# Performance work log

Measured on AMD Instinct MI355X. Metric: run time of the kernel, lower is better.

The kernel has to match this reference:

```python
import jax, jax.numpy as jnp
import numpy as np

MARGIN = 1.0
EPS = 1e-6


def _cos(a, b):
    # Row-wise cosine similarity, matching torch.nn.CosineSimilarity semantics:
    # dot / max(||a|| * ||b||, eps)
    num = jnp.sum(a * b, axis=-1)
    den = jnp.maximum(jnp.linalg.norm(a, axis=-1) * jnp.linalg.norm(b, axis=-1), EPS)
    return num / den


def setup_inputs() -> dict:
    key = jax.random.key(0)
    k1, k2, k3 = jax.random.split(key, 3)
    B, D = 16384, 1024
    output = jax.random.normal(k1, (B, D), dtype=jnp.float32)
    target = jax.random.normal(k2, (B, D), dtype=jnp.float32)
    # offset in [0, B-1); j = (i + 1 + neg_idx) % B guarantees j != i, uniform over the rest
    neg_idx = jax.random.randint(k3, (B,), 0, B - 1, dtype=jnp.int64)
    return {"output": output, "target": target, "neg_idx": neg_idx}


def reference(output, target, neg_idx):
    B = output.shape[0]
    j = (jnp.arange(B) + 1 + neg_idx) % B  # random negative index, j != i
    t_neg = target[j]                       # gather negative label embeddings [B, D]
    hinge = jax.nn.relu(MARGIN - _cos(target, output) + _cos(t_neg, output))
    return jnp.sum(hinge) / B
```

## Files before the change

### kernel.cpp

```cpp
#include <hip/hip_runtime.h>
#include <hip/hip_bf16.h>


#define EPS 1e-6f

typedef float f4 __attribute__((ext_vector_type(4)));

#define DPP_STEP(x, ctrl, rm, bm)                                             \
    x += __int_as_float(__builtin_amdgcn_update_dpp(                          \
        0, __float_as_int(x), (ctrl), (rm), (bm), true))

__device__ __forceinline__ float dpp_wave_sum(float x) {
    DPP_STEP(x, 0x111, 0xf, 0xf);
    DPP_STEP(x, 0x112, 0xf, 0xf);
    DPP_STEP(x, 0x114, 0xf, 0xe);
    DPP_STEP(x, 0x118, 0xf, 0xc);
    DPP_STEP(x, 0x142, 0xa, 0xf);
    DPP_STEP(x, 0x143, 0xc, 0xf);
    return x;
}

struct RowBuf {
    f4 o[4], t[4], n[4];
};

__device__ __forceinline__ void issue_loads(RowBuf& rb,
                                            const float* __restrict__ outm,
                                            const float* __restrict__ tgt,
                                            int i, int j, int lane, int D) {
    const f4* o4 = (const f4*)(outm + (size_t)i * D);
    const f4* t4 = (const f4*)(tgt  + (size_t)i * D);
    const f4* n4 = (const f4*)(tgt  + (size_t)j * D);
#pragma unroll
    for (int k = 0; k < 4; ++k)
        rb.o[k] = __builtin_nontemporal_load(&o4[lane + 64 * k]);
#pragma unroll
    for (int k = 0; k < 4; ++k) rb.t[k] = t4[lane + 64 * k];
#pragma unroll
    for (int k = 0; k < 4; ++k) rb.n[k] = n4[lane + 64 * k];
}

__device__ __forceinline__ float consume(const RowBuf& rb) {
    float dto = 0.f, dno = 0.f, oo = 0.f, tt = 0.f, nn = 0.f;
#pragma unroll
    for (int k = 0; k < 4; ++k) {
        dto += rb.o[k].x*rb.t[k].x + rb.o[k].y*rb.t[k].y + rb.o[k].z*rb.t[k].z + rb.o[k].w*rb.t[k].w;
        dno += rb.o[k].x*rb.n[k].x + rb.o[k].y*rb.n[k].y + rb.o[k].z*rb.n[k].z + rb.o[k].w*rb.n[k].w;
        oo  += rb.o[k].x*rb.o[k].x + rb.o[k].y*rb.o[k].y + rb.o[k].z*rb.o[k].z + rb.o[k].w*rb.o[k].w;
        tt  += rb.t[k].x*rb.t[k].x + rb.t[k].y*rb.t[k].y + rb.t[k].z*rb.t[k].z + rb.t[k].w*rb.t[k].w;
        nn  += rb.n[k].x*rb.n[k].x + rb.n[k].y*rb.n[k].y + rb.n[k].z*rb.n[k].z + rb.n[k].w*rb.n[k].w;
    }
    dto = dpp_wave_sum(dto);
    dno = dpp_wave_sum(dno);
    oo  = dpp_wave_sum(oo);
    tt  = dpp_wave_sum(tt);
    nn  = dpp_wave_sum(nn);
    float no = sqrtf(oo);
    float h  = 1.f - dto / fmaxf(sqrtf(tt) * no, EPS)
                   + dno / fmaxf(sqrtf(nn) * no, EPS);
    return fmaxf(h, 0.f);
}

__global__ __launch_bounds__(256, 4) void hinge_cos_kernel(
    const float* __restrict__ outm,
    const float* __restrict__ tgt,
    const int*   __restrict__ negidx,
    float* __restrict__ res,
    int B, int D, float invB) {

    const int lane  = threadIdx.x & 63;
    const int wave  = threadIdx.x >> 6;
    const int wpb   = blockDim.x >> 6;
    const int gwave = blockIdx.x * wpb + wave;
    const int nwav  = gridDim.x * wpb;

    float acc = 0.f;

    RowBuf cur, nxt;
    int i = gwave;
    if (i < B) {
        int j = i + 1 + negidx[i];
        if (j >= B) j -= B;
        issue_loads(cur, outm, tgt, i, j, lane, D);
    }
    while (i < B) {
        const int inext = i + nwav;
        const bool havenext = inext < B;
        if (havenext) {
            int jn = inext + 1 + negidx[inext];
            if (jn >= B) jn -= B;
            issue_loads(nxt, outm, tgt, inext, jn, lane, D);
        }
        float h = consume(cur);
        if (lane == 63) acc += h;
        if (havenext) cur = nxt;
        i = inext;
    }

    __shared__ float red[4];
    if (lane == 63) red[wave] = acc;
    __syncthreads();
    if (threadIdx.x == 0) {
        float s = 0.f;
#pragma unroll
        for (int w = 0; w < 4; ++w) s += red[w];
        atomicAdd(res, s * invB);
    }
}

extern "C" void kernel_launch(void* const* d_in, const int* in_sizes, int n_in,
                              void* d_out, int out_size, void* d_ws, size_t ws_size,
                              hipStream_t stream) {
    const float* outm   = (const float*)d_in[0];
    const float* tgt    = (const float*)d_in[1];
    const int*   negidx = (const int*)d_in[2];
    float* res = (float*)d_out;

    const int B = in_sizes[2];
    const int D = in_sizes[0] / B;

    (void)hipMemsetAsync(res, 0, sizeof(float), stream);

    hinge_cos_kernel<<<1024, 256, 0, stream>>>(outm, tgt, negidx, res, B, D,
                                               1.0f / (float)B);
}
```

Measured before the change: 141.9 us.

## Replace register double-buffering with higher occupancy and prefetched neg index

Drops the explicit next-row register double buffer and instead loads the current row's vectors directly, prefetching only the next negative index. This cuts register pressure, which allows launch bounds of 8 blocks per CU and a grid of 2048 blocks, so more waves hide memory latency. The trade-off is that each wave no longer overlaps its own next-row loads with the current compute, and relies on the hardware scheduler across more waves instead. The scalar hinge math is now limited to lane 63.

```diff
diff --git a/kernel.cpp b/kernel.cpp
--- a/kernel.cpp
+++ b/kernel.cpp
@@ -20,48 +20,7 @@
     return x;
 }
 
-struct RowBuf {
-    f4 o[4], t[4], n[4];
-};
-
-__device__ __forceinline__ void issue_loads(RowBuf& rb,
-                                            const float* __restrict__ outm,
-                                            const float* __restrict__ tgt,
-                                            int i, int j, int lane, int D) {
-    const f4* o4 = (const f4*)(outm + (size_t)i * D);
-    const f4* t4 = (const f4*)(tgt  + (size_t)i * D);
-    const f4* n4 = (const f4*)(tgt  + (size_t)j * D);
-#pragma unroll
-    for (int k = 0; k < 4; ++k)
-        rb.o[k] = __builtin_nontemporal_load(&o4[lane + 64 * k]);
-#pragma unroll
-    for (int k = 0; k < 4; ++k) rb.t[k] = t4[lane + 64 * k];
-#pragma unroll
-    for (int k = 0; k < 4; ++k) rb.n[k] = n4[lane + 64 * k];
-}
-
-__device__ __forceinline__ float consume(const RowBuf& rb) {
-    float dto = 0.f, dno = 0.f, oo = 0.f, tt = 0.f, nn = 0.f;
-#pragma unroll
-    for (int k = 0; k < 4; ++k) {
-        dto += rb.o[k].x*rb.t[k].x + rb.o[k].y*rb.t[k].y + rb.o[k].z*rb.t[k].z + rb.o[k].w*rb.t[k].w;
-        dno += rb.o[k].x*rb.n[k].x + rb.o[k].y*rb.n[k].y + rb.o[k].z*rb.n[k].z + rb.o[k].w*rb.n[k].w;
-        oo  += rb.o[k].x*rb.o[k].x + rb.o[k].y*rb.o[k].y + rb.o[k].z*rb.o[k].z + rb.o[k].w*rb.o[k].w;
-        tt  += rb.t[k].x*rb.t[k].x + rb.t[k].y*rb.t[k].y + rb.t[k].z*rb.t[k].z + rb.t[k].w*rb.t[k].w;
-        nn  += rb.n[k].x*rb.n[k].x + rb.n[k].y*rb.n[k].y + rb.n[k].z*rb.n[k].z + rb.n[k].w*rb.n[k].w;
-    }
-    dto = dpp_wave_sum(dto);
-    dno = dpp_wave_sum(dno);
-    oo  = dpp_wave_sum(oo);
-    tt  = dpp_wave_sum(tt);
-    nn  = dpp_wave_sum(nn);
-    float no = sqrtf(oo);
-    float h  = 1.f - dto / fmaxf(sqrtf(tt) * no, EPS)
-                   + dno / fmaxf(sqrtf(nn) * no, EPS);
-    return fmaxf(h, 0.f);
-}
-
-__global__ __launch_bounds__(256, 4) void hinge_cos_kernel(
+__global__ __launch_bounds__(256, 8) void hinge_cos_kernel(
     const float* __restrict__ outm,
     const float* __restrict__ tgt,
     const int*   __restrict__ negidx,
@@ -70,30 +29,64 @@
 
     const int lane  = threadIdx.x & 63;
     const int wave  = threadIdx.x >> 6;
-    const int wpb   = blockDim.x >> 6;
-    const int gwave = blockIdx.x * wpb + wave;
-    const int nwav  = gridDim.x * wpb;
+    const int gwave = blockIdx.x * 4 + wave;
+    const int nwav  = gridDim.x * 4;
 
     float acc = 0.f;
 
-    RowBuf cur, nxt;
     int i = gwave;
+    int jcur = 0;
     if (i < B) {
-        int j = i + 1 + negidx[i];
-        if (j >= B) j -= B;
-        issue_loads(cur, outm, tgt, i, j, lane, D);
+        jcur = i + 1 + negidx[i];
+        if (jcur >= B) jcur -= B;
     }
+
     while (i < B) {
         const int inext = i + nwav;
-        const bool havenext = inext < B;
-        if (havenext) {
-            int jn = inext + 1 + negidx[inext];
-            if (jn >= B) jn -= B;
-            issue_loads(nxt, outm, tgt, inext, jn, lane, D);
+
+        int jn_raw = 0;
+        if (inext < B) jn_raw = negidx[inext];
+
+        const f4* o4 = (const f4*)(outm + (size_t)i * D);
+        const f4* t4 = (const f4*)(tgt  + (size_t)i * D);
+        const f4* n4 = (const f4*)(tgt  + (size_t)jcur * D);
+
+        f4 o[4], t[4], n[4];
+#pragma unroll
+        for (int k = 0; k < 4; ++k)
+            o[k] = __builtin_nontemporal_load(&o4[lane + 64 * k]);
+#pragma unroll
+        for (int k = 0; k < 4; ++k) t[k] = t4[lane + 64 * k];
+#pragma unroll
+        for (int k = 0; k < 4; ++k) n[k] = n4[lane + 64 * k];
+
+        int jnext = inext + 1 + jn_raw;
+        if (jnext >= B) jnext -= B;
+
+        float dto = 0.f, dno = 0.f, oo = 0.f, tt = 0.f, nn = 0.f;
+#pragma unroll
+        for (int k = 0; k < 4; ++k) {
+            dto += o[k].x*t[k].x + o[k].y*t[k].y + o[k].z*t[k].z + o[k].w*t[k].w;
+            dno += o[k].x*n[k].x + o[k].y*n[k].y + o[k].z*n[k].z + o[k].w*n[k].w;
+            oo  += o[k].x*o[k].x + o[k].y*o[k].y + o[k].z*o[k].z + o[k].w*o[k].w;
+            tt  += t[k].x*t[k].x + t[k].y*t[k].y + t[k].z*t[k].z + t[k].w*t[k].w;
+            nn  += n[k].x*n[k].x + n[k].y*n[k].y + n[k].z*n[k].z + n[k].w*n[k].w;
         }
-        float h = consume(cur);
-        if (lane == 63) acc += h;
-        if (havenext) cur = nxt;
+
+        dto = dpp_wave_sum(dto);
+        dno = dpp_wave_sum(dno);
+        oo  = dpp_wave_sum(oo);
+        tt  = dpp_wave_sum(tt);
+        nn  = dpp_wave_sum(nn);
+
+        if (lane == 63) {
+            float no = sqrtf(oo);
+            float h  = 1.f - dto / fmaxf(sqrtf(tt) * no, EPS)
+                           + dno / fmaxf(sqrtf(nn) * no, EPS);
+            acc += fmaxf(h, 0.f);
+        }
+
+        jcur = jnext;
         i = inext;
     }
 
@@ -121,6 +114,6 @@
 
     (void)hipMemsetAsync(res, 0, sizeof(float), stream);
 
-    hinge_cos_kernel<<<1024, 256, 0, stream>>>(outm, tgt, negidx, res, B, D,
+    hinge_cos_kernel<<<2048, 256, 0, stream>>>(outm, tgt, negidx, res, B, D,
                                                1.0f / (float)B);
 }
```

Result: slower. 152.5 us (+7.5%).
